# Optimization experiments

Hardware: AMD Instinct MI355X
Metric: run time of the kernel (lower is better)

## Reference

```python
import jax, jax.numpy as jnp
import numpy as np

N, D, R, E = 10000, 1024, 8, 80000


def setup_inputs() -> dict:
    key = jax.random.key(0)
    ks = jax.random.split(key, 8)
    s = 1.0 / np.sqrt(D)
    x = jax.random.normal(ks[0], (N, D), dtype=jnp.float32)
    edge_index = jax.random.randint(ks[1], (2, E), 0, N, dtype=jnp.int64)
    edge_type = jax.random.randint(ks[2], (E,), 0, R, dtype=jnp.int64)
    weight = jax.random.normal(ks[3], (R, D, D), dtype=jnp.float32) * s  # per-relation W_r
    root = jax.random.normal(ks[4], (D, D), dtype=jnp.float32) * s      # root/self-loop weight
    bias = jnp.zeros((D,), dtype=jnp.float32)
    w_gate = jax.random.normal(ks[5], (2 * D, D), dtype=jnp.float32) * (1.0 / np.sqrt(2 * D))
    b_gate = jnp.zeros((D,), dtype=jnp.float32)
    return {"x": x, "edge_index": edge_index, "edge_type": edge_type,
            "weight": weight, "root": root, "bias": bias,
            "w_gate": w_gate, "b_gate": b_gate}


def _rgcn(x, edge_index, edge_type, weight, root, bias):
    # PyG RGCNConv (aggr='mean'): per relation r, mean-aggregate x[src] into dst,
    # then transform by W_r (aggregate-then-transform, equivalent by linearity).
    src, dst = edge_index[0], edge_index[1]
    msgs = x[src]                                   # [E, D] gather
    out = x @ root + bias                           # root/self connection
    n = x.shape[0]
    for r in range(weight.shape[0]):                # small fixed relation loop
        mask = (edge_type == r).astype(x.dtype)     # [E]
        sums = jax.ops.segment_sum(msgs * mask[:, None], dst, num_segments=n)
        cnt = jax.ops.segment_sum(mask, dst, num_segments=n)
        mean = sums / jnp.maximum(cnt, 1.0)[:, None]
        out = out + mean @ weight[r]
    return out


def reference(x, edge_index, edge_type, weight, root, bias, w_gate, b_gate):
    u = _rgcn(x, edge_index, edge_type, weight, root, bias)
    # dropout p=0 -> identity
    z = jnp.concatenate([u, x], axis=1) @ w_gate + b_gate
    h = jnp.tanh(u) * z + x * (1.0 - z)
    return h
```

## Files before the change

### kernel.cpp

```cpp
#include <hip/hip_runtime.h>
#include <math.h>

typedef unsigned short u16;
typedef __attribute__((ext_vector_type(8))) short bf16x8;
typedef __attribute__((ext_vector_type(4))) float f32x4;

static constexpr int kN = 10000;
static constexpr int kNpad = 10240;
static constexpr int kD = 1024;
static constexpr int kR = 8;
static constexpr int kE = 80000;
static constexpr int kKz = 2 * kD;
static constexpr int kCrows = kNpad * (kR + 1);

#define GLB(p) ((const __attribute__((address_space(1))) unsigned int*)(const void*)(p))
#define LDSP(p) ((__attribute__((address_space(3))) unsigned int*)(p))

__device__ __forceinline__ u16 f2bf(float f) {
    union { float f; unsigned int i; } c; c.f = f;
    unsigned int u = c.i;
    return (u16)((u + 0x7FFFu + ((u >> 16) & 1u)) >> 16);
}
__device__ __forceinline__ float bf2f(u16 u) {
    union { unsigned int i; float f; } c; c.i = ((unsigned int)u) << 16;
    return c.f;
}
__device__ __forceinline__ ushort4 f2bf4(float4 v) {
    ushort4 o; o.x = f2bf(v.x); o.y = f2bf(v.y); o.z = f2bf(v.z); o.w = f2bf(v.w);
    return o;
}

__global__ void zero16(uint4* __restrict__ p, long n16) {
    long i = (long)blockIdx.x * blockDim.x + threadIdx.x;
    long st = (long)gridDim.x * blockDim.x;
    uint4 z = make_uint4(0, 0, 0, 0);
    for (; i < n16; i += st) p[i] = z;
}

__global__ void mark_edges(const int* __restrict__ src, const int* __restrict__ dst,
                           const int* __restrict__ etype,
                           int* __restrict__ cntd, int* __restrict__ flag) {
    int e = blockIdx.x * blockDim.x + threadIdx.x;
    if (e < kE) {
        atomicAdd(&cntd[dst[e]], 1);
        flag[etype[e] * kN + src[e]] = 1;
    }
}

__global__ __launch_bounds__(1024) void scan_rowptr(const int* __restrict__ cnt,
                                                    int* __restrict__ rowptr,
                                                    int* __restrict__ cursor) {
    __shared__ int wsum[16];
    __shared__ int carry;
    const int tid = threadIdx.x;
    const int lane = tid & 63;
    const int w = tid >> 6;
    if (tid == 0) carry = 0;
    const int nchunk = (kN + 1024) / 1024;
    for (int ch = 0; ch < nchunk; ++ch) {
        int idx = ch * 1024 + tid;
        int v = (idx < kN) ? cnt[idx] : 0;
        int s = v;
#pragma unroll
        for (int off = 1; off < 64; off <<= 1) {
            int t = __shfl_up(s, off, 64);
            if (lane >= off) s += t;
        }
        if (lane == 63) wsum[w] = s;
        __syncthreads();
        if (w == 0 && lane < 16) {
            int t = wsum[lane];
#pragma unroll
            for (int off = 1; off < 16; off <<= 1) {
                int tt = __shfl_up(t, off, 64);
                if (lane >= off) t += tt;
            }
            wsum[lane] = t;
        }
        __syncthreads();
        int wpre = (w > 0) ? wsum[w - 1] : 0;
        int incl = s + wpre + carry;
        int excl = incl - v;
        if (idx <= kN) rowptr[idx] = excl;
        if (idx < kN) cursor[idx] = 0;
        __syncthreads();
        if (tid == 1023) carry = incl;
        __syncthreads();
    }
}

__global__ __launch_bounds__(1024) void compact_scan(const int* __restrict__ flag,
                                                     int* __restrict__ row_src,
                                                     int* __restrict__ pos_tab,
                                                     int* __restrict__ relcnt9) {
    const int tid = threadIdx.x;
    if (blockIdx.x == kR) {
        for (int i = tid; i < kNpad; i += 1024) row_src[i] = i;
        if (tid == 0) relcnt9[0] = kN;
        return;
    }
    const int r = blockIdx.x;
    const int base = kNpad * (r + 1);
    __shared__ int wsum[16];
    __shared__ int carry;
    const int lane = tid & 63;
    const int w = tid >> 6;
    if (tid == 0) carry = 0;
    const int nchunk = (kN + 1023) / 1024;
    for (int ch = 0; ch < nchunk; ++ch) {
        int idx = ch * 1024 + tid;
        int v = (idx < kN) ? flag[r * kN + idx] : 0;
        int s = v;
#pragma unroll
        for (int off = 1; off < 64; off <<= 1) {
            int t = __shfl_up(s, off, 64);
            if (lane >= off) s += t;
        }
        if (lane == 63) wsum[w] = s;
        __syncthreads();
        if (w == 0 && lane < 16) {
            int t = wsum[lane];
#pragma unroll
            for (int off = 1; off < 16; off <<= 1) {
                int tt = __shfl_up(t, off, 64);
                if (lane >= off) t += tt;
            }
            wsum[lane] = t;
        }
        __syncthreads();
        int wpre = (w > 0) ? wsum[w - 1] : 0;
        int incl = s + wpre + carry;
        int excl = incl - v;
        if (idx < kN && v) {
            row_src[base + excl] = idx;
            pos_tab[r * kN + idx] = base + excl;
        }
        __syncthreads();
        if (tid == 1023) carry = incl;
        __syncthreads();
    }
    if (tid == 0) relcnt9[r + 1] = carry;
}

__global__ void fill_edges(const int* __restrict__ src, const int* __restrict__ dst,
                           const int* __restrict__ etype, const int* __restrict__ rowptr,
                           int* __restrict__ cursor, const int* __restrict__ pos_tab,
                           int* __restrict__ erec) {
    int e = blockIdx.x * blockDim.x + threadIdx.x;
    if (e < kE) {
        int d = dst[e], r = etype[e], s = src[e];
        int pos = rowptr[d] + atomicAdd(&cursor[d], 1);
        erec[pos] = (pos_tab[r * kN + s] << 3) | r;
    }
}

__global__ void cvt_x(const float* __restrict__ x, u16* __restrict__ ga) {
    int row = blockIdx.x;
    int c = threadIdx.x << 2;
    float4 v = *reinterpret_cast<const float4*>(x + (size_t)row * kD + c);
    *reinterpret_cast<ushort4*>(ga + (size_t)row * kKz + kD + c) = f2bf4(v);
}

__global__ void transpose_to_bf16(const float* __restrict__ S, u16* __restrict__ D,
                                  int rows, int cols, int ldD) {
    S += (size_t)blockIdx.z * rows * cols;
    D += (size_t)blockIdx.z * rows * cols;
    __shared__ float t[32][33];
    int c0 = blockIdx.x * 32, r0 = blockIdx.y * 32;
    int x = threadIdx.x, y = threadIdx.y;
#pragma unroll
    for (int i = 0; i < 32; i += 8)
        t[y + i][x] = S[(size_t)(r0 + y + i) * cols + c0 + x];
    __syncthreads();
#pragma unroll
    for (int i = 0; i < 32; i += 8)
        D[(size_t)(c0 + y + i) * ldD + r0 + x] = f2bf(t[x][y + i]);
}

__global__ __launch_bounds__(256) void aggregate(const u16* __restrict__ yc,
                                                 const float* __restrict__ bias,
                                                 const int* __restrict__ rowptr,
                                                 const int* __restrict__ erec,
                                                 u16* __restrict__ ga) {
    const int d = blockIdx.x;
    const int c = threadIdx.x << 2;
    const int e0 = rowptr[d], e1 = rowptr[d + 1];

    __shared__ float rs[kR];
    if (threadIdx.x == 0) {
        int cc[kR] = {0, 0, 0, 0, 0, 0, 0, 0};
        for (int e = e0; e < e1; ++e) cc[erec[e] & 7]++;
#pragma unroll
        for (int r = 0; r < kR; ++r) rs[r] = 1.0f / fmaxf((float)cc[r], 1.0f);
    }
    __syncthreads();

    ushort4 rv = *reinterpret_cast<const ushort4*>(yc + (size_t)d * kD + c);
    float4 bv = *reinterpret_cast<const float4*>(bias + c);
    float4 acc = make_float4(bf2f(rv.x) + bv.x, bf2f(rv.y) + bv.y,
                             bf2f(rv.z) + bv.z, bf2f(rv.w) + bv.w);

    int e = e0;
    for (; e + 3 < e1; e += 4) {
        int rec0 = erec[e], rec1 = erec[e + 1], rec2 = erec[e + 2], rec3 = erec[e + 3];
        ushort4 v0 = *reinterpret_cast<const ushort4*>(yc + (size_t)(rec0 >> 3) * kD + c);
        ushort4 v1 = *reinterpret_cast<const ushort4*>(yc + (size_t)(rec1 >> 3) * kD + c);
        ushort4 v2 = *reinterpret_cast<const ushort4*>(yc + (size_t)(rec2 >> 3) * kD + c);
        ushort4 v3 = *reinterpret_cast<const ushort4*>(yc + (size_t)(rec3 >> 3) * kD + c);
        float s0 = rs[rec0 & 7], s1 = rs[rec1 & 7], s2 = rs[rec2 & 7], s3 = rs[rec3 & 7];
        acc.x += s0 * bf2f(v0.x); acc.y += s0 * bf2f(v0.y);
        acc.z += s0 * bf2f(v0.z); acc.w += s0 * bf2f(v0.w);
        acc.x += s1 * bf2f(v1.x); acc.y += s1 * bf2f(v1.y);
        acc.z += s1 * bf2f(v1.z); acc.w += s1 * bf2f(v1.w);
        acc.x += s2 * bf2f(v2.x); acc.y += s2 * bf2f(v2.y);
        acc.z += s2 * bf2f(v2.z); acc.w += s2 * bf2f(v2.w);
        acc.x += s3 * bf2f(v3.x); acc.y += s3 * bf2f(v3.y);
        acc.z += s3 * bf2f(v3.z); acc.w += s3 * bf2f(v3.w);
    }
    for (; e < e1; ++e) {
        int rec = erec[e];
        float sc = rs[rec & 7];
        ushort4 v = *reinterpret_cast<const ushort4*>(yc + (size_t)(rec >> 3) * kD + c);
        acc.x += sc * bf2f(v.x); acc.y += sc * bf2f(v.y);
        acc.z += sc * bf2f(v.z); acc.w += sc * bf2f(v.w);
    }
    *reinterpret_cast<ushort4*>(ga + (size_t)d * kKz + c) = f2bf4(acc);
}

__global__ __launch_bounds__(512, 2) void gemm_compact(
    const u16* __restrict__ xb, int ldx,
    const u16* __restrict__ Bt9,
    const int* __restrict__ row_src, const int* __restrict__ relcnt9,
    u16* __restrict__ yc)
{
    const int t0 = blockIdx.y;
    const int relidx = t0 / 40;
    const int lt = t0 - relidx * 40;
    if (lt * 256 >= relcnt9[relidx]) return;

    __shared__ u16 sA[2][256 * 64];
    __shared__ u16 sB[2][256 * 64];

    const int tid = threadIdx.x;
    const int wave = tid >> 6;
    const int lane = tid & 63;

    const int row0 = t0 * 256;
    const int col0 = blockIdx.x * 256;

    const int s_row = tid >> 3;
    const int s_src = ((tid & 7) ^ (s_row & 7)) * 8;
    const int wbase = wave * 512;

    const u16* gA[4];
    const u16* gB[4];
#pragma unroll
    for (int q = 0; q < 4; ++q) {
        gA[q] = xb + (size_t)row_src[row0 + q * 64 + s_row] * ldx + s_src;
        gB[q] = Bt9 + (size_t)(relidx * kD + col0 + q * 64 + s_row) * kD + s_src;
    }

    auto stage = [&](int b) {
        u16* dA = &sA[b][0];
        u16* dB = &sB[b][0];
#pragma unroll
        for (int q = 0; q < 4; ++q) {
            __builtin_amdgcn_global_load_lds(GLB(gA[q]), LDSP(dA + q * 4096 + wbase), 16, 0, 0);
            gA[q] += 64;
        }
#pragma unroll
        for (int q = 0; q < 4; ++q) {
            __builtin_amdgcn_global_load_lds(GLB(gB[q]), LDSP(dB + q * 4096 + wbase), 16, 0, 0);
            gB[q] += 64;
        }
    };

    const int wm = (wave >> 2) * 128;
    const int wn = (wave & 3) * 64;
    const int fm = lane & 15;
    const int g4 = lane >> 4;
    const int pc0 = ((g4) ^ (fm & 7)) * 8;
    const int pc1 = ((4 | g4) ^ (fm & 7)) * 8;

    f32x4 zf = {0.0f, 0.0f, 0.0f, 0.0f};
    f32x4 acc[8][4];
#pragma unroll
    for (int i = 0; i < 8; ++i)
#pragma unroll
        for (int j = 0; j < 4; ++j) acc[i][j] = zf;

    constexpr int T = kD / 64;
    stage(0);
    stage(1);

    for (int t = 0; t < T; ++t) {
        if (t + 1 < T) asm volatile("s_waitcnt vmcnt(8)" ::: "memory");
        else           asm volatile("s_waitcnt vmcnt(0)" ::: "memory");
        __builtin_amdgcn_s_barrier();
        asm volatile("" ::: "memory");

        const u16* cA = sA[t & 1];
        const u16* cB = sB[t & 1];
        bf16x8 af[8], bfv[4];

#pragma unroll
        for (int i = 0; i < 8; ++i)
            af[i] = *reinterpret_cast<const bf16x8*>(&cA[(wm + i * 16 + fm) * 64 + pc0]);
#pragma unroll
        for (int j = 0; j < 4; ++j)
            bfv[j] = *reinterpret_cast<const bf16x8*>(&cB[(wn + j * 16 + fm) * 64 + pc0]);
        __builtin_amdgcn_s_setprio(1);
#pragma unroll
        for (int i = 0; i < 8; ++i)
#pragma unroll
            for (int j = 0; j < 4; ++j)
                acc[i][j] = __builtin_amdgcn_mfma_f32_16x16x32_bf16(bfv[j], af[i], acc[i][j], 0, 0, 0);
        __builtin_amdgcn_s_setprio(0);

#pragma unroll
        for (int i = 0; i < 8; ++i)
            af[i] = *reinterpret_cast<const bf16x8*>(&cA[(wm + i * 16 + fm) * 64 + pc1]);
#pragma unroll
        for (int j = 0; j < 4; ++j)
            bfv[j] = *reinterpret_cast<const bf16x8*>(&cB[(wn + j * 16 + fm) * 64 + pc1]);
        __builtin_amdgcn_s_setprio(1);
#pragma unroll
        for (int i = 0; i < 8; ++i)
#pragma unroll
            for (int j = 0; j < 4; ++j)
                acc[i][j] = __builtin_amdgcn_mfma_f32_16x16x32_bf16(bfv[j], af[i], acc[i][j], 0, 0, 0);
        __builtin_amdgcn_s_setprio(0);

        asm volatile("" ::: "memory");
        __builtin_amdgcn_s_barrier();
        if (t + 2 < T) stage(t & 1);
    }

    const int cq = g4 * 4;
#pragma unroll
    for (int i = 0; i < 8; ++i) {
        int row = row0 + wm + i * 16 + fm;
#pragma unroll
        for (int j = 0; j < 4; ++j) {
            int col = col0 + wn + j * 16 + cq;
            f32x4 v = acc[i][j];
            ushort4 o;
            o.x = f2bf(v[0]); o.y = f2bf(v[1]); o.z = f2bf(v[2]); o.w = f2bf(v[3]);
            *reinterpret_cast<ushort4*>(yc + (size_t)row * kD + col) = o;
        }
    }
}

__global__ __launch_bounds__(256, 3) void gemm_mfma_gate(
    const u16* __restrict__ A, int lda,
    const u16* __restrict__ Bt, int ldb, int K,
    int M, const float* __restrict__ bias,
    float* __restrict__ Cf, const u16* __restrict__ uga, const float* __restrict__ xo)
{
    __shared__ u16 sA[3][128 * 32];
    __shared__ u16 sB[3][128 * 32];

    const int tid = threadIdx.x;
    const int wave = tid >> 6;
    const int lane = tid & 63;

    constexpr int GX = kD / 128;
    constexpr int GY = kNpad / 128;
    const int lin = blockIdx.y * GX + blockIdx.x;
    const int xcd = lin & 7;
    const int pos = lin >> 3;
    const int ty = xcd * (GY / 8) + (pos >> 3);
    const int tx = pos & 7;

    const int row0 = ty * 128;
    const int col0 = tx * 128;

    const int srow = wave * 16 + (lane >> 2);
    const int scol = (((lane & 3) ^ ((srow >> 1) & 3)) * 8);

    const u16* gA0 = A + (size_t)(row0 + srow) * lda + scol;
    const u16* gA1 = A + (size_t)(row0 + 64 + srow) * lda + scol;
    const u16* gB0 = Bt + (size_t)(col0 + srow) * ldb + scol;
    const u16* gB1 = Bt + (size_t)(col0 + 64 + srow) * ldb + scol;

    const int lof0 = (wave * 16) * 32;
    const int lof1 = (64 + wave * 16) * 32;

    const int mq = (wave >> 1) * 64;
    const int nq = (wave & 1) * 64;
    const int fm = lane & 15;
    const int fkx = (((lane >> 4) ^ ((fm >> 1) & 3))) * 8;

    f32x4 zf = {0.0f, 0.0f, 0.0f, 0.0f};
    f32x4 acc[4][4];
#pragma unroll
    for (int i = 0; i < 4; ++i)
#pragma unroll
        for (int j = 0; j < 4; ++j) acc[i][j] = zf;

    auto stage = [&](int s) {
        __builtin_amdgcn_global_load_lds(GLB(gA0), LDSP(sA[s] + lof0), 16, 0, 0);
        __builtin_amdgcn_global_load_lds(GLB(gA1), LDSP(sA[s] + lof1), 16, 0, 0);
        __builtin_amdgcn_global_load_lds(GLB(gB0), LDSP(sB[s] + lof0), 16, 0, 0);
        __builtin_amdgcn_global_load_lds(GLB(gB1), LDSP(sB[s] + lof1), 16, 0, 0);
        gA0 += 32; gA1 += 32; gB0 += 32; gB1 += 32;
    };

    const int T = K >> 5;
    stage(0);
    stage(1);

    int s = 0;
    for (int t = 0; t < T; ++t) {
        if (t + 2 < T) {
            stage(s == 0 ? 2 : (s - 1));
            asm volatile("s_waitcnt vmcnt(8)" ::: "memory");
        } else if (t + 1 < T) {
            asm volatile("s_waitcnt vmcnt(4)" ::: "memory");
        } else {
            asm volatile("s_waitcnt vmcnt(0)" ::: "memory");
        }
        __builtin_amdgcn_s_barrier();
        asm volatile("" ::: "memory");

        const u16* cA = sA[s];
        const u16* cB = sB[s];
        bf16x8 af[4], bfr[4];
#pragma unroll
        for (int i = 0; i < 4; ++i)
            af[i] = *reinterpret_cast<const bf16x8*>(&cA[(mq + i * 16 + fm) * 32 + fkx]);
#pragma unroll
        for (int j = 0; j < 4; ++j)
            bfr[j] = *reinterpret_cast<const bf16x8*>(&cB[(nq + j * 16 + fm) * 32 + fkx]);
#pragma unroll
        for (int i = 0; i < 4; ++i)
#pragma unroll
            for (int j = 0; j < 4; ++j)
                acc[i][j] = __builtin_amdgcn_mfma_f32_16x16x32_bf16(bfr[j], af[i], acc[i][j], 0, 0, 0);

        asm volatile("" ::: "memory");
        __builtin_amdgcn_s_barrier();
        s = (s == 2) ? 0 : (s + 1);
    }

    const int cq = (lane >> 4) * 4;
#pragma unroll
    for (int i = 0; i < 4; ++i) {
        int row = row0 + mq + i * 16 + fm;
        if (row >= M) continue;
#pragma unroll
        for (int j = 0; j < 4; ++j) {
            int col = col0 + nq + j * 16 + cq;
            f32x4 v = acc[i][j];
            float4 bv = *reinterpret_cast<const float4*>(bias + col);
            v[0] += bv.x; v[1] += bv.y; v[2] += bv.z; v[3] += bv.w;
            ushort4 ur = *reinterpret_cast<const ushort4*>(uga + (size_t)row * kKz + col);
            float4 xr = *reinterpret_cast<const float4*>(xo + (size_t)row * kD + col);
            float4 h;
            h.x = tanhf(bf2f(ur.x)) * v[0] + xr.x * (1.0f - v[0]);
            h.y = tanhf(bf2f(ur.y)) * v[1] + xr.y * (1.0f - v[1]);
            h.z = tanhf(bf2f(ur.z)) * v[2] + xr.z * (1.0f - v[2]);
            h.w = tanhf(bf2f(ur.w)) * v[3] + xr.w * (1.0f - v[3]);
            *reinterpret_cast<float4*>(Cf + (size_t)row * kD + col) = h;
        }
    }
}

extern "C" void kernel_launch(void* const* d_in, const int* in_sizes, int n_in,
                              void* d_out, int out_size, void* d_ws, size_t ws_size,
                              hipStream_t stream) {
    (void)in_sizes; (void)n_in; (void)out_size; (void)ws_size;

    const float* x     = (const float*)d_in[0];
    const int* eidx    = (const int*)d_in[1];
    const int* etype   = (const int*)d_in[2];
    const float* weight= (const float*)d_in[3];
    const float* root  = (const float*)d_in[4];
    const float* bias  = (const float*)d_in[5];
    const float* wgate = (const float*)d_in[6];
    const float* bgate = (const float*)d_in[7];
    float* out = (float*)d_out;

    const int* src = eidx;
    const int* dst = eidx + kE;

    char* ws = (char*)d_ws;
    size_t off = 0;
    u16* yc   = (u16*)(ws + off);    off += (size_t)kCrows * kD * 2;
    u16* ga   = (u16*)(ws + off);    off += (size_t)kNpad * kKz * 2;
    u16* Bt9  = (u16*)(ws + off);    off += (size_t)(kR + 1) * kD * kD * 2;
    u16* wg_t = (u16*)(ws + off);    off += (size_t)kD * kKz * 2;
    int* cntd    = (int*)(ws + off); off += (size_t)kN * 4;
    int* flag    = (int*)(ws + off); off += (size_t)kR * kN * 4;
    int* row_src = (int*)(ws + off); off += (size_t)kCrows * 4;
    int* pos_tab = (int*)(ws + off); off += (size_t)kR * kN * 4;
    int* rowp    = (int*)(ws + off); off += (size_t)(kN + 16) * 4;
    int* curs    = (int*)(ws + off); off += (size_t)kN * 4;
    int* erec    = (int*)(ws + off); off += (size_t)kE * 4;
    int* relcnt9 = (int*)(ws + off); off += 16 * 4;

    zero16<<<180, 256, 0, stream>>>((uint4*)cntd, (long)(kN + kR * kN + kCrows) / 4);

    mark_edges<<<(kE + 255) / 256, 256, 0, stream>>>(src, dst, etype, cntd, flag);
    scan_rowptr<<<1, 1024, 0, stream>>>(cntd, rowp, curs);
    compact_scan<<<kR + 1, 1024, 0, stream>>>(flag, row_src, pos_tab, relcnt9);
    fill_edges<<<(kE + 255) / 256, 256, 0, stream>>>(src, dst, etype, rowp, curs,
                                                     pos_tab, erec);

    zero16<<<256, 256, 0, stream>>>((uint4*)(ga + (size_t)kN * kKz),
                                    (long)(kNpad - kN) * kKz * 2 / 16);

    cvt_x<<<kN, 256, 0, stream>>>(x, ga);

    {
        dim3 b(32, 8);
        transpose_to_bf16<<<dim3(kD / 32, kD / 32, 1), b, 0, stream>>>(root, Bt9, kD, kD, kD);
        transpose_to_bf16<<<dim3(kD / 32, kD / 32, kR), b, 0, stream>>>(
            weight, Bt9 + (size_t)kD * kD, kD, kD, kD);
        transpose_to_bf16<<<dim3(kD / 32, kKz / 32, 1), b, 0, stream>>>(wgate, wg_t, kKz, kD, kKz);
    }

    dim3 g1(kD / 256, kCrows / 256);
    gemm_compact<<<g1, 512, 0, stream>>>(ga + kD, kKz, Bt9, row_src, relcnt9, yc);

    aggregate<<<kN, 256, 0, stream>>>(yc, bias, rowp, erec, ga);

    dim3 g2(kD / 128, kNpad / 128);
    gemm_mfma_gate<<<g2, 256, 0, stream>>>(ga, kKz, wg_t, kKz, kKz, kN, bgate, out, ga, x);
}
```

Measured before the change: 478.0 us.

## Interleave half-tile global-to-LDS loads with quadrant MFMA phases in RGCN GEMM

Restructures the main GEMM loop into four compute phases, one per quadrant of the warp's output tile. Each phase issues a half-tile of A or B global-to-LDS prefetch for the next buffer, separated by barriers, so loads are interleaved with MFMA work instead of issued in one block at loop end. Fragments are reused across phases to cut LDS reads. This adds barriers per iteration and changes the vmcnt accounting, which could cost more than the overlap gains.

```diff
diff --git a/kernel.cpp b/kernel.cpp
--- a/kernel.cpp
+++ b/kernel.cpp
@@ -260,16 +260,18 @@
         gB[q] = Bt9 + (size_t)(relidx * kD + col0 + q * 64 + s_row) * kD + s_src;
     }
 
-    auto stage = [&](int b) {
+    auto stageA = [&](int b, int h) {
         u16* dA = &sA[b][0];
-        u16* dB = &sB[b][0];
-#pragma unroll
-        for (int q = 0; q < 4; ++q) {
+#pragma unroll
+        for (int q = 2 * h; q < 2 * h + 2; ++q) {
             __builtin_amdgcn_global_load_lds(GLB(gA[q]), LDSP(dA + q * 4096 + wbase), 16, 0, 0);
             gA[q] += 64;
         }
-#pragma unroll
-        for (int q = 0; q < 4; ++q) {
+    };
+    auto stageB = [&](int b, int h) {
+        u16* dB = &sB[b][0];
+#pragma unroll
+        for (int q = 2 * h; q < 2 * h + 2; ++q) {
             __builtin_amdgcn_global_load_lds(GLB(gB[q]), LDSP(dB + q * 4096 + wbase), 16, 0, 0);
             gB[q] += 64;
         }
@@ -290,50 +292,92 @@
         for (int j = 0; j < 4; ++j) acc[i][j] = zf;
 
     constexpr int T = kD / 64;
-    stage(0);
-    stage(1);
+    stageA(0, 0); stageB(0, 0); stageB(0, 1); stageA(0, 1);
+
+    bf16x8 af[8], bfl[4], bfh[4];
 
     for (int t = 0; t < T; ++t) {
-        if (t + 1 < T) asm volatile("s_waitcnt vmcnt(8)" ::: "memory");
-        else           asm volatile("s_waitcnt vmcnt(0)" ::: "memory");
+        const int cb = t & 1, nb = cb ^ 1;
+        const bool pf = (t + 1 < T);
+        const u16* cA = sA[cb];
+        const u16* cB = sB[cb];
+
+        if (pf) {
+            stageA(nb, 0);
+            asm volatile("s_waitcnt vmcnt(2)" ::: "memory");
+        } else {
+            asm volatile("s_waitcnt vmcnt(0)" ::: "memory");
+        }
         __builtin_amdgcn_s_barrier();
         asm volatile("" ::: "memory");
-
-        const u16* cA = sA[t & 1];
-        const u16* cB = sB[t & 1];
-        bf16x8 af[8], bfv[4];
-
-#pragma unroll
-        for (int i = 0; i < 8; ++i)
-            af[i] = *reinterpret_cast<const bf16x8*>(&cA[(wm + i * 16 + fm) * 64 + pc0]);
-#pragma unroll
-        for (int j = 0; j < 4; ++j)
-            bfv[j] = *reinterpret_cast<const bf16x8*>(&cB[(wn + j * 16 + fm) * 64 + pc0]);
+#pragma unroll
+        for (int i = 0; i < 4; ++i) {
+            af[2 * i]     = *reinterpret_cast<const bf16x8*>(&cA[(wm + i * 16 + fm) * 64 + pc0]);
+            af[2 * i + 1] = *reinterpret_cast<const bf16x8*>(&cA[(wm + i * 16 + fm) * 64 + pc1]);
+        }
+#pragma unroll
+        for (int j = 0; j < 2; ++j) {
+            bfl[2 * j]     = *reinterpret_cast<const bf16x8*>(&cB[(wn + j * 16 + fm) * 64 + pc0]);
+            bfl[2 * j + 1] = *reinterpret_cast<const bf16x8*>(&cB[(wn + j * 16 + fm) * 64 + pc1]);
+        }
         __builtin_amdgcn_s_setprio(1);
 #pragma unroll
-        for (int i = 0; i < 8; ++i)
-#pragma unroll
-            for (int j = 0; j < 4; ++j)
-                acc[i][j] = __builtin_amdgcn_mfma_f32_16x16x32_bf16(bfv[j], af[i], acc[i][j], 0, 0, 0);
+        for (int i = 0; i < 4; ++i)
+#pragma unroll
+            for (int j = 0; j < 2; ++j) {
+                acc[i][j] = __builtin_amdgcn_mfma_f32_16x16x32_bf16(bfl[2 * j], af[2 * i], acc[i][j], 0, 0, 0);
+                acc[i][j] = __builtin_amdgcn_mfma_f32_16x16x32_bf16(bfl[2 * j + 1], af[2 * i + 1], acc[i][j], 0, 0, 0);
+            }
         __builtin_amdgcn_s_setprio(0);
 
-#pragma unroll
-        for (int i = 0; i < 8; ++i)
-            af[i] = *reinterpret_cast<const bf16x8*>(&cA[(wm + i * 16 + fm) * 64 + pc1]);
-#pragma unroll
-        for (int j = 0; j < 4; ++j)
-            bfv[j] = *reinterpret_cast<const bf16x8*>(&cB[(wn + j * 16 + fm) * 64 + pc1]);
+        if (pf) stageB(nb, 0);
+        __builtin_amdgcn_s_barrier();
+        asm volatile("" ::: "memory");
+#pragma unroll
+        for (int j = 0; j < 2; ++j) {
+            bfh[2 * j]     = *reinterpret_cast<const bf16x8*>(&cB[(wn + 32 + j * 16 + fm) * 64 + pc0]);
+            bfh[2 * j + 1] = *reinterpret_cast<const bf16x8*>(&cB[(wn + 32 + j * 16 + fm) * 64 + pc1]);
+        }
         __builtin_amdgcn_s_setprio(1);
 #pragma unroll
-        for (int i = 0; i < 8; ++i)
-#pragma unroll
-            for (int j = 0; j < 4; ++j)
-                acc[i][j] = __builtin_amdgcn_mfma_f32_16x16x32_bf16(bfv[j], af[i], acc[i][j], 0, 0, 0);
+        for (int i = 0; i < 4; ++i)
+#pragma unroll
+            for (int j = 0; j < 2; ++j) {
+                acc[i][2 + j] = __builtin_amdgcn_mfma_f32_16x16x32_bf16(bfh[2 * j], af[2 * i], acc[i][2 + j], 0, 0, 0);
+                acc[i][2 + j] = __builtin_amdgcn_mfma_f32_16x16x32_bf16(bfh[2 * j + 1], af[2 * i + 1], acc[i][2 + j], 0, 0, 0);
+            }
         __builtin_amdgcn_s_setprio(0);
 
+        if (pf) stageB(nb, 1);
+        __builtin_amdgcn_s_barrier();
         asm volatile("" ::: "memory");
+#pragma unroll
+        for (int i = 0; i < 4; ++i) {
+            af[2 * i]     = *reinterpret_cast<const bf16x8*>(&cA[(wm + 64 + i * 16 + fm) * 64 + pc0]);
+            af[2 * i + 1] = *reinterpret_cast<const bf16x8*>(&cA[(wm + 64 + i * 16 + fm) * 64 + pc1]);
+        }
+        __builtin_amdgcn_s_setprio(1);
+#pragma unroll
+        for (int i = 0; i < 4; ++i)
+#pragma unroll
+            for (int j = 0; j < 2; ++j) {
+                acc[4 + i][2 + j] = __builtin_amdgcn_mfma_f32_16x16x32_bf16(bfh[2 * j], af[2 * i], acc[4 + i][2 + j], 0, 0, 0);
+                acc[4 + i][2 + j] = __builtin_amdgcn_mfma_f32_16x16x32_bf16(bfh[2 * j + 1], af[2 * i + 1], acc[4 + i][2 + j], 0, 0, 0);
+            }
+        __builtin_amdgcn_s_setprio(0);
+
+        if (pf) stageA(nb, 1);
         __builtin_amdgcn_s_barrier();
-        if (t + 2 < T) stage(t & 1);
+        asm volatile("" ::: "memory");
+        __builtin_amdgcn_s_setprio(1);
+#pragma unroll
+        for (int i = 0; i < 4; ++i)
+#pragma unroll
+            for (int j = 0; j < 2; ++j) {
+                acc[4 + i][j] = __builtin_amdgcn_mfma_f32_16x16x32_bf16(bfl[2 * j], af[2 * i], acc[4 + i][j], 0, 0, 0);
+                acc[4 + i][j] = __builtin_amdgcn_mfma_f32_16x16x32_bf16(bfl[2 * j + 1], af[2 * i + 1], acc[4 + i][j], 0, 0, 0);
+            }
+        __builtin_amdgcn_s_setprio(0);
     }
 
     const int cq = g4 * 4;
```

Result: no change. 469.6 us (-1.8%).
